# Optimization experiments

Hardware: AMD Instinct MI355X
Metric: run time of the kernel (lower is better)

Reference implementation:

```python
import jax, jax.numpy as jnp
import numpy as np

B = 8192       # batch
HID = 1024     # hidden_dim
HEADS = 8      # head_count
OBS, ACT, N_AGENTS = 128, 32, 4
ENC_IN = N_AGENTS * OBS + ACT   # 544
DEC_IN = (N_AGENTS - 1) * ACT   # 96


def _linear(key, fan_in, fan_out):
    k1, k2 = jax.random.split(key)
    lim = 1.0 / np.sqrt(fan_in)
    W = jax.random.uniform(k1, (fan_in, fan_out), minval=-lim, maxval=lim, dtype=jnp.float32)
    b = jax.random.uniform(k2, (fan_out,), minval=-lim, maxval=lim, dtype=jnp.float32)
    return W, b


def setup_inputs() -> dict:
    key = jax.random.key(0)
    ks = jax.random.split(key, 10)
    s = jax.random.normal(ks[0], (B, N_AGENTS * OBS), dtype=jnp.float32)
    a = jax.random.normal(ks[1], (B, N_AGENTS * ACT), dtype=jnp.float32)
    W_enc_in, b_enc_in = _linear(ks[2], ENC_IN, HID)   # encoder_input_fc
    W_dec_in, b_dec_in = _linear(ks[3], DEC_IN, HID)   # decoder_input_fc
    W_eh, b_eh = _linear(ks[4], HID, HID)              # fc_encoder_input
    head_ks = jax.random.split(ks[5], HEADS)
    Wb = [_linear(k, HID, HID) for k in head_ks]       # fc_encoder_heads
    W_heads = jnp.stack([w for w, _ in Wb], axis=0)    # [H, HID, HID]
    b_heads = jnp.stack([b for _, b in Wb], axis=0)    # [H, HID]
    W_dh, b_dh = _linear(ks[6], HID, HID)              # fc_decoder_input
    W1, b1 = _linear(ks[7], HID, HID)                  # fc1
    W2, b2 = _linear(ks[8], HID, 1)                    # fc2
    return {"s": s, "a": a,
            "W_enc_in": W_enc_in, "b_enc_in": b_enc_in,
            "W_dec_in": W_dec_in, "b_dec_in": b_dec_in,
            "W_eh": W_eh, "b_eh": b_eh,
            "W_heads": W_heads, "b_heads": b_heads,
            "W_dh": W_dh, "b_dh": b_dh,
            "W1": W1, "b1": b1, "W2": W2, "b2": b2}


def reference(s, a, W_enc_in, b_enc_in, W_dec_in, b_dec_in, W_eh, b_eh,
              W_heads, b_heads, W_dh, b_dh, W1, b1, W2, b2):
    relu = jax.nn.relu
    # agent id = 0: own action is a[:, :ACT], others' actions are a[:, ACT:]
    enc_input = jnp.concatenate([s, a[:, :ACT]], axis=1) @ W_enc_in + b_enc_in   # [B, HID]
    dec_input = a[:, ACT:] @ W_dec_in + b_dec_in                                 # [B, HID]
    # Attention_ATT_2
    encoder_h = relu(enc_input @ W_eh + b_eh)                                    # [B, HID]
    encoder_heads = relu(jnp.einsum('bd,hde->hbe', encoder_h, W_heads)
                         + b_heads[:, None, :])                                  # [H, B, HID]
    decoder_H = relu(dec_input @ W_dh + b_dh)                                    # [B, HID]
    scores = jnp.einsum('hbd,bd->bh', encoder_heads, decoder_H)                  # [B, H]
    attn = jax.nn.softmax(scores, axis=1)                                        # [B, H]
    context = jnp.einsum('hbd,bh->bd', encoder_heads, attn)                      # [B, HID]
    x = relu(context @ W1 + b1)
    q = x @ W2 + b2                                                              # [B, 1]
    return q
```

## Files before the change

kernel.cpp:

```cpp
#include <hip/hip_runtime.h>
#include <hip/hip_bf16.h>
#include <hip/hip_fp16.h>

#define BATCH   8192
#define HID     1024
#define HEADS   8
#define BC      2048

typedef unsigned int  u32;
typedef unsigned short u16;
typedef __attribute__((ext_vector_type(8))) short bf16x8;
typedef __attribute__((ext_vector_type(4))) float f32x4;

__device__ __forceinline__ u32 pack_hi2(u32 u0, u32 u1) {
    return (u0 >> 16) | (u1 & 0xFFFF0000u);
}
__device__ __forceinline__ void split1(float x, u16& h, u16& l) {
    const u32 u = __float_as_uint(x);
    h = (u16)(u >> 16);
    const float r = x - __uint_as_float(u & 0xFFFF0000u);
    l = (u16)(__float_as_uint(r) >> 16);
}
__device__ __forceinline__ void splitA4(float4 v, uint2& hi, uint2& lo) {
    u32 u0 = __float_as_uint(v.x), u1 = __float_as_uint(v.y),
        u2 = __float_as_uint(v.z), u3 = __float_as_uint(v.w);
    float r0 = v.x - __uint_as_float(u0 & 0xFFFF0000u);
    float r1 = v.y - __uint_as_float(u1 & 0xFFFF0000u);
    float r2 = v.z - __uint_as_float(u2 & 0xFFFF0000u);
    float r3 = v.w - __uint_as_float(u3 & 0xFFFF0000u);
    hi.x = pack_hi2(u0, u1);
    hi.y = pack_hi2(u2, u3);
    lo.x = pack_hi2(__float_as_uint(r0), __float_as_uint(r1));
    lo.y = pack_hi2(__float_as_uint(r2), __float_as_uint(r3));
}

__device__ __forceinline__ void gld16(const u16* g, u16* l) {
    __builtin_amdgcn_global_load_lds(
        (const __attribute__((address_space(1))) u32*)g,
        (__attribute__((address_space(3))) u32*)l, 16, 0, 0);
}

__global__ __launch_bounds__(256) void split_weight_kernel(
    const float* __restrict__ W, u16* __restrict__ hi, u16* __restrict__ lo,
    int K)
{
    const long long zoff = (long long)blockIdx.z * K * 1024;
    const int kt  = blockIdx.x;
    const int n0  = blockIdx.y * 128;
    const int tid = threadIdx.x;
    const int k   = tid >> 3;
    const int ng  = (tid & 7) * 16;
    const float* src = W + zoff + (long long)(kt * 32 + k) * 1024 + n0 + ng;
    u16* dh = hi + zoff + ((long long)kt * 1024 + n0) * 32 + k;
    u16* dl = lo + zoff + ((long long)kt * 1024 + n0) * 32 + k;
#pragma unroll
    for (int t = 0; t < 4; t++) {
        const float4 v = *(const float4*)(src + t * 4);
        u16 h0, l0, h1, l1, h2, l2, h3, l3;
        split1(v.x, h0, l0); split1(v.y, h1, l1);
        split1(v.z, h2, l2); split1(v.w, h3, l3);
        const int nb = (ng + t * 4) * 32;
        dh[nb]      = h0; dl[nb]      = l0;
        dh[nb + 32] = h1; dl[nb + 32] = l1;
        dh[nb + 64] = h2; dl[nb + 64] = l2;
        dh[nb + 96] = h3; dl[nb + 96] = l3;
    }
}

#define MFMA_GEOM \
    const int tid  = threadIdx.x; \
    const int lane = tid & 63; \
    const int wv   = tid >> 6; \
    const int wm   = wv >> 1, wn = wv & 1; \
    const int fr   = lane & 15; \
    const int fq   = lane >> 4; \
    const int fqx  = (fq ^ (fr & 3)) * 8; \
    const int lro  = (lane >> 2) * 32 + (((lane & 3) ^ ((lane >> 2) & 3)) * 8); \
    const int br0  = wv * 16; \
    const int br1  = 64 + wv * 16;

template <int RELU, int OUTP>
__global__ __launch_bounds__(256) void gemm_fast(
    const u16* __restrict__ Ahp, const u16* __restrict__ Alp, int MA, int moff,
    const u16* __restrict__ Bhp, const u16* __restrict__ Blp,
    const float* __restrict__ bias,
    float* __restrict__ Cf,
    u16* __restrict__ Chp, u16* __restrict__ Clp, int MC,
    int K)
{
    __shared__ alignas(16) u16 Ah[4096], Al[4096], Bh[4096], Bl[4096];
    MFMA_GEOM
    const int m0 = blockIdx.y * 128;
    const int n0 = blockIdx.x * 128;

    f32x4 acc[4][4];
#pragma unroll
    for (int i = 0; i < 4; i++)
#pragma unroll
        for (int j = 0; j < 4; j++) acc[i][j] = 0;

    const int KT = K >> 5;
    for (int kt = 0; kt < KT; kt++) {
        const u16* Ag  = Ahp + ((long long)kt * MA + moff + m0) * 32;
        const u16* Ag2 = Alp + ((long long)kt * MA + moff + m0) * 32;
        const u16* Bg  = Bhp + ((long long)kt * 1024 + n0) * 32;
        const u16* Bg2 = Blp + ((long long)kt * 1024 + n0) * 32;
        gld16(Ag  + br0 * 32 + lro, &Ah[br0 * 32]);
        gld16(Ag  + br1 * 32 + lro, &Ah[br1 * 32]);
        gld16(Ag2 + br0 * 32 + lro, &Al[br0 * 32]);
        gld16(Ag2 + br1 * 32 + lro, &Al[br1 * 32]);
        gld16(Bg  + br0 * 32 + lro, &Bh[br0 * 32]);
        gld16(Bg  + br1 * 32 + lro, &Bh[br1 * 32]);
        gld16(Bg2 + br0 * 32 + lro, &Bl[br0 * 32]);
        gld16(Bg2 + br1 * 32 + lro, &Bl[br1 * 32]);
        __syncthreads();

        bf16x8 ah[4], al[4], bh[4], bl[4];
#pragma unroll
        for (int i = 0; i < 4; i++) {
            const int off = (wm * 64 + i * 16 + fr) * 32 + fqx;
            ah[i] = *(const bf16x8*)&Ah[off];
            al[i] = *(const bf16x8*)&Al[off];
        }
#pragma unroll
        for (int j = 0; j < 4; j++) {
            const int off = (wn * 64 + j * 16 + fr) * 32 + fqx;
            bh[j] = *(const bf16x8*)&Bh[off];
            bl[j] = *(const bf16x8*)&Bl[off];
        }
#pragma unroll
        for (int i = 0; i < 4; i++)
#pragma unroll
            for (int j = 0; j < 4; j++) {
                acc[i][j] = __builtin_amdgcn_mfma_f32_16x16x32_bf16(ah[i], bh[j], acc[i][j], 0, 0, 0);
                acc[i][j] = __builtin_amdgcn_mfma_f32_16x16x32_bf16(ah[i], bl[j], acc[i][j], 0, 0, 0);
                acc[i][j] = __builtin_amdgcn_mfma_f32_16x16x32_bf16(al[i], bh[j], acc[i][j], 0, 0, 0);
            }
        __syncthreads();
    }

#pragma unroll
    for (int j = 0; j < 4; j++) {
        const int n = n0 + wn * 64 + j * 16 + fr;
        const float bb = bias[n];
#pragma unroll
        for (int i = 0; i < 4; i++) {
#pragma unroll
            for (int r = 0; r < 4; r++) {
                const int m = m0 + wm * 64 + i * 16 + fq * 4 + r;
                float v = acc[i][j][r] + bb;
                if (RELU) v = fmaxf(v, 0.0f);
                if (OUTP) {
                    u16 h, l;
                    split1(v, h, l);
                    const long long d = ((long long)(n >> 5) * MC + moff + m) * 32 + (n & 31);
                    Chp[d] = h;
                    Clp[d] = l;
                } else {
                    Cf[(long long)m * 1024 + n] = v;
                }
            }
        }
    }
}

template <int RELU>
__global__ __launch_bounds__(256) void gemm_cvt(
    const float* __restrict__ src1, int lda1, int kofs1,
    const float* __restrict__ src2, int lda2, int ksplit,
    const u16* __restrict__ Bhp, const u16* __restrict__ Blp,
    const float* __restrict__ bias,
    u16* __restrict__ Chp, u16* __restrict__ Clp, int MC,
    int K)
{
    __shared__ alignas(16) u16 Ah[4096], Al[4096], Bh[4096], Bl[4096];
    MFMA_GEOM
    const int m0  = blockIdx.y * 128;
    const int n0  = blockIdx.x * 128;
    const int ar  = tid >> 3;
    const int akq = tid & 7;
    const int awoff = (( (akq >> 1) ^ (ar & 3) ) * 8) + (akq & 1) * 4;

    f32x4 acc[4][4];
#pragma unroll
    for (int i = 0; i < 4; i++)
#pragma unroll
        for (int j = 0; j < 4; j++) acc[i][j] = 0;

    const int KT = K >> 5;
    for (int kt = 0; kt < KT; kt++) {
        const int k0 = kt * 32;
        const float* srcp; int ldk, kc;
        if (k0 < ksplit) { srcp = src1; ldk = lda1; kc = k0 + kofs1; }
        else             { srcp = src2; ldk = lda2; kc = k0 - ksplit; }

        const u16* Bg  = Bhp + ((long long)kt * 1024 + n0) * 32;
        const u16* Bg2 = Blp + ((long long)kt * 1024 + n0) * 32;
        gld16(Bg  + br0 * 32 + lro, &Bh[br0 * 32]);
        gld16(Bg  + br1 * 32 + lro, &Bh[br1 * 32]);
        gld16(Bg2 + br0 * 32 + lro, &Bl[br0 * 32]);
        gld16(Bg2 + br1 * 32 + lro, &Bl[br1 * 32]);

#pragma unroll
        for (int it = 0; it < 4; it++) {
            const int row = ar + it * 32;
            const float4 v = *(const float4*)(srcp + (long long)(m0 + row) * ldk + kc + akq * 4);
            uint2 hi, lo;
            splitA4(v, hi, lo);
            *(uint2*)&Ah[row * 32 + awoff] = hi;
            *(uint2*)&Al[row * 32 + awoff] = lo;
        }
        __syncthreads();

        bf16x8 ah[4], al[4], bh[4], bl[4];
#pragma unroll
        for (int i = 0; i < 4; i++) {
            const int off = (wm * 64 + i * 16 + fr) * 32 + fqx;
            ah[i] = *(const bf16x8*)&Ah[off];
            al[i] = *(const bf16x8*)&Al[off];
        }
#pragma unroll
        for (int j = 0; j < 4; j++) {
            const int off = (wn * 64 + j * 16 + fr) * 32 + fqx;
            bh[j] = *(const bf16x8*)&Bh[off];
            bl[j] = *(const bf16x8*)&Bl[off];
        }
#pragma unroll
        for (int i = 0; i < 4; i++)
#pragma unroll
            for (int j = 0; j < 4; j++) {
                acc[i][j] = __builtin_amdgcn_mfma_f32_16x16x32_bf16(ah[i], bh[j], acc[i][j], 0, 0, 0);
                acc[i][j] = __builtin_amdgcn_mfma_f32_16x16x32_bf16(ah[i], bl[j], acc[i][j], 0, 0, 0);
                acc[i][j] = __builtin_amdgcn_mfma_f32_16x16x32_bf16(al[i], bh[j], acc[i][j], 0, 0, 0);
            }
        __syncthreads();
    }

#pragma unroll
    for (int j = 0; j < 4; j++) {
        const int n = n0 + wn * 64 + j * 16 + fr;
        const float bb = bias[n];
#pragma unroll
        for (int i = 0; i < 4; i++) {
#pragma unroll
            for (int r = 0; r < 4; r++) {
                const int m = m0 + wm * 64 + i * 16 + fq * 4 + r;
                float v = acc[i][j][r] + bb;
                if (RELU) v = fmaxf(v, 0.0f);
                u16 h, l;
                split1(v, h, l);
                const long long d = ((long long)(n >> 5) * MC + m) * 32 + (n & 31);
                Chp[d] = h;
                Clp[d] = l;
            }
        }
    }
}

__global__ __launch_bounds__(256) void heads_kernel(
    const u16* __restrict__ Ahp, const u16* __restrict__ Alp, int MA, int moff,
    const u16* __restrict__ Whp, const u16* __restrict__ Wlp,
    const float* __restrict__ b_heads,
    const float* __restrict__ decH,
    __half* __restrict__ headsb,
    float* __restrict__ scoresp)
{
    __shared__ alignas(16) u16 Ah[4096], Al[4096], Bh[4096], Bl[4096];
    __shared__ float scred[2][128];
    MFMA_GEOM
    const int h = blockIdx.z;
    const u16* Bhp = Whp + (long long)h * 1024 * 1024;
    const u16* Blp = Wlp + (long long)h * 1024 * 1024;
    const float* bias = b_heads + h * 1024;
    const int m0 = blockIdx.y * 128;
    const int n0 = blockIdx.x * 128;

    f32x4 acc[4][4];
#pragma unroll
    for (int i = 0; i < 4; i++)
#pragma unroll
        for (int j = 0; j < 4; j++) acc[i][j] = 0;

    for (int kt = 0; kt < 32; kt++) {
        const u16* Ag  = Ahp + ((long long)kt * MA + moff + m0) * 32;
        const u16* Ag2 = Alp + ((long long)kt * MA + moff + m0) * 32;
        const u16* Bg  = Bhp + ((long long)kt * 1024 + n0) * 32;
        const u16* Bg2 = Blp + ((long long)kt * 1024 + n0) * 32;
        gld16(Ag  + br0 * 32 + lro, &Ah[br0 * 32]);
        gld16(Ag  + br1 * 32 + lro, &Ah[br1 * 32]);
        gld16(Ag2 + br0 * 32 + lro, &Al[br0 * 32]);
        gld16(Ag2 + br1 * 32 + lro, &Al[br1 * 32]);
        gld16(Bg  + br0 * 32 + lro, &Bh[br0 * 32]);
        gld16(Bg  + br1 * 32 + lro, &Bh[br1 * 32]);
        gld16(Bg2 + br0 * 32 + lro, &Bl[br0 * 32]);
        gld16(Bg2 + br1 * 32 + lro, &Bl[br1 * 32]);
        __syncthreads();

        bf16x8 ah[4], al[4], bh[4], bl[4];
#pragma unroll
        for (int i = 0; i < 4; i++) {
            const int off = (wm * 64 + i * 16 + fr) * 32 + fqx;
            ah[i] = *(const bf16x8*)&Ah[off];
            al[i] = *(const bf16x8*)&Al[off];
        }
#pragma unroll
        for (int j = 0; j < 4; j++) {
            const int off = (wn * 64 + j * 16 + fr) * 32 + fqx;
            bh[j] = *(const bf16x8*)&Bh[off];
            bl[j] = *(const bf16x8*)&Bl[off];
        }
#pragma unroll
        for (int i = 0; i < 4; i++)
#pragma unroll
            for (int j = 0; j < 4; j++) {
                acc[i][j] = __builtin_amdgcn_mfma_f32_16x16x32_bf16(ah[i], bh[j], acc[i][j], 0, 0, 0);
                acc[i][j] = __builtin_amdgcn_mfma_f32_16x16x32_bf16(ah[i], bl[j], acc[i][j], 0, 0, 0);
                acc[i][j] = __builtin_amdgcn_mfma_f32_16x16x32_bf16(al[i], bh[j], acc[i][j], 0, 0, 0);
            }
        __syncthreads();
    }

    float part[4][4];
#pragma unroll
    for (int i = 0; i < 4; i++)
#pragma unroll
        for (int r = 0; r < 4; r++) part[i][r] = 0.0f;

#pragma unroll
    for (int j = 0; j < 4; j++) {
        const int n = n0 + wn * 64 + j * 16 + fr;
        const float bb = bias[n];
#pragma unroll
        for (int i = 0; i < 4; i++) {
#pragma unroll
            for (int r = 0; r < 4; r++) {
                const int b_loc = m0 + wm * 64 + i * 16 + fq * 4 + r;
                const float v = fmaxf(acc[i][j][r] + bb, 0.0f);
                headsb[((long long)b_loc * HEADS + h) * 1024 + n] = __float2half(v);
                part[i][r] = fmaf(v, decH[(long long)b_loc * 1024 + n], part[i][r]);
            }
        }
    }
#pragma unroll
    for (int off = 1; off < 16; off <<= 1)
#pragma unroll
        for (int i = 0; i < 4; i++)
#pragma unroll
            for (int r = 0; r < 4; r++)
                part[i][r] += __shfl_xor(part[i][r], off, 64);

    if (fr == 0) {
#pragma unroll
        for (int i = 0; i < 4; i++)
#pragma unroll
            for (int r = 0; r < 4; r++)
                scred[wn][wm * 64 + i * 16 + fq * 4 + r] = part[i][r];
    }
    __syncthreads();
    if (tid < 128) {
        const float sv = scred[0][tid] + scred[1][tid];
        scoresp[(long long)(h * 8 + blockIdx.x) * BC + m0 + tid] = sv;
    }
}

__global__ __launch_bounds__(256) void softmax_kernel(
    const float* __restrict__ scoresp, float* __restrict__ attn)
{
    const int b = blockIdx.x * 256 + threadIdx.x;
    float sc[HEADS];
#pragma unroll
    for (int h = 0; h < HEADS; h++) {
        float s = 0.0f;
#pragma unroll
        for (int nt = 0; nt < 8; nt++)
            s += scoresp[(long long)(h * 8 + nt) * BC + b];
        sc[h] = s;
    }
    float mx = sc[0];
#pragma unroll
    for (int h = 1; h < HEADS; h++) mx = fmaxf(mx, sc[h]);
    float e[HEADS], sum = 0.0f;
#pragma unroll
    for (int h = 0; h < HEADS; h++) { e[h] = __expf(sc[h] - mx); sum += e[h]; }
    const float inv = 1.0f / sum;
#pragma unroll
    for (int h = 0; h < HEADS; h++) attn[(long long)b * HEADS + h] = e[h] * inv;
}

__global__ __launch_bounds__(256) void context_kernel(
    const __half* __restrict__ headsb, const float* __restrict__ attn,
    u16* __restrict__ ctx_hi, u16* __restrict__ ctx_lo, int MC, int row0)
{
    const int b = blockIdx.x;
    const int d = threadIdx.x * 4;
    float w[HEADS];
#pragma unroll
    for (int h = 0; h < HEADS; h++) w[h] = attn[(long long)b * HEADS + h];
    float4 acc = make_float4(0.f, 0.f, 0.f, 0.f);
#pragma unroll
    for (int h = 0; h < HEADS; h++) {
        const __half2* hp = (const __half2*)(headsb + ((long long)b * HEADS + h) * 1024 + d);
        const float2 f0 = __half22float2(hp[0]);
        const float2 f1 = __half22float2(hp[1]);
        acc.x = fmaf(w[h], f0.x, acc.x);
        acc.y = fmaf(w[h], f0.y, acc.y);
        acc.z = fmaf(w[h], f1.x, acc.z);
        acc.w = fmaf(w[h], f1.y, acc.w);
    }
    uint2 hi, lo;
    splitA4(acc, hi, lo);
    const long long off = ((long long)(d >> 5) * MC + row0 + b) * 32 + (d & 31);
    *(uint2*)(ctx_hi + off) = hi;
    *(uint2*)(ctx_lo + off) = lo;
}

__global__ __launch_bounds__(256) void fc2_kernel(
    const float* __restrict__ x, const float* __restrict__ W2,
    const float* __restrict__ b2, float* __restrict__ q)
{
    const int b   = blockIdx.x;
    const int tid = threadIdx.x;
    __shared__ float red[4];

    const float4 xv = *(const float4*)(x + (long long)b * 1024 + tid * 4);
    const float4 wv = *(const float4*)(W2 + tid * 4);
    float p = xv.x * wv.x + xv.y * wv.y + xv.z * wv.z + xv.w * wv.w;
#pragma unroll
    for (int off = 32; off > 0; off >>= 1) p += __shfl_down(p, off, 64);
    if ((tid & 63) == 0) red[tid >> 6] = p;
    __syncthreads();
    if (tid == 0) q[b] = red[0] + red[1] + red[2] + red[3] + b2[0];
}

extern "C" void kernel_launch(void* const* d_in, const int* in_sizes, int n_in,
                              void* d_out, int out_size, void* d_ws, size_t ws_size,
                              hipStream_t stream)
{
    const float* s        = (const float*)d_in[0];
    const float* a        = (const float*)d_in[1];
    const float* W_enc_in = (const float*)d_in[2];
    const float* b_enc_in = (const float*)d_in[3];
    const float* W_dec_in = (const float*)d_in[4];
    const float* b_dec_in = (const float*)d_in[5];
    const float* W_eh     = (const float*)d_in[6];
    const float* b_eh     = (const float*)d_in[7];
    const float* W_heads  = (const float*)d_in[8];
    const float* b_heads  = (const float*)d_in[9];
    const float* W_dh     = (const float*)d_in[10];
    const float* b_dh     = (const float*)d_in[11];
    const float* W1       = (const float*)d_in[12];
    const float* b1       = (const float*)d_in[13];
    const float* W2       = (const float*)d_in[14];
    const float* b2       = (const float*)d_in[15];
    float* q_out = (float*)d_out;

    u16* P = (u16*)d_ws;
    u16* enc_hi = P; P += 557056;
    u16* enc_lo = P; P += 557056;
    u16* dec_hi = P; P += 98304;
    u16* dec_lo = P; P += 98304;
    u16* eh_hi  = P; P += 1048576;
    u16* eh_lo  = P; P += 1048576;
    u16* dh_hi  = P; P += 1048576;
    u16* dh_lo  = P; P += 1048576;
    u16* w1_hi  = P; P += 1048576;
    u16* w1_lo  = P; P += 1048576;
    u16* wh_hi  = P; P += 8388608;
    u16* wh_lo  = P; P += 8388608;
    char* act = (char*)P;

    const dim3 blk(256);

    split_weight_kernel<<<dim3(17, 8, 1), blk, 0, stream>>>(W_enc_in, enc_hi, enc_lo, 544);
    split_weight_kernel<<<dim3(3, 8, 1), blk, 0, stream>>>(W_dec_in, dec_hi, dec_lo, 96);
    split_weight_kernel<<<dim3(32, 8, 1), blk, 0, stream>>>(W_eh, eh_hi, eh_lo, 1024);
    split_weight_kernel<<<dim3(32, 8, 1), blk, 0, stream>>>(W_dh, dh_hi, dh_lo, 1024);
    split_weight_kernel<<<dim3(32, 8, 1), blk, 0, stream>>>(W1, w1_hi, w1_lo, 1024);
    split_weight_kernel<<<dim3(32, 8, 8), blk, 0, stream>>>(W_heads, wh_hi, wh_lo, 1024);

    const bool high = (ws_size >= 150011904ULL);

    if (high) {
        u16*    bufA_hi = (u16*)act;
        u16*    bufA_lo = bufA_hi + 8388608;
        __half* headsb  = (__half*)act;
        u16*    encH_hi = (u16*)(act + 33554432);
        u16*    encH_lo = encH_hi + 8388608;
        float*  decH    = (float*)(act + 2LL * 33554432);
        float*  scoresp = (float*)(act + 3LL * 33554432);
        float*  attnb   = scoresp + 64LL * BC;

        const dim3 gg(8, 64, 1);
        gemm_cvt<0><<<gg, blk, 0, stream>>>(s, 512, 0, a, 128, 512,
            enc_hi, enc_lo, b_enc_in, bufA_hi, bufA_lo, 8192, 544);
        gemm_fast<1, 1><<<gg, blk, 0, stream>>>(bufA_hi, bufA_lo, 8192, 0,
            eh_hi, eh_lo, b_eh, nullptr, encH_hi, encH_lo, 8192, 1024);
        gemm_cvt<0><<<gg, blk, 0, stream>>>(a, 128, 32, a, 128, 1 << 28,
            dec_hi, dec_lo, b_dec_in, bufA_hi, bufA_lo, 8192, 96);
        gemm_fast<1, 0><<<gg, blk, 0, stream>>>(bufA_hi, bufA_lo, 8192, 0,
            dh_hi, dh_lo, b_dh, decH, nullptr, nullptr, 0, 1024);

        for (int c = 0; c < BATCH / BC; c++) {
            heads_kernel<<<dim3(8, BC / 128, 8), blk, 0, stream>>>(
                encH_hi, encH_lo, 8192, c * BC, wh_hi, wh_lo, b_heads,
                decH + (long long)c * BC * 1024, headsb, scoresp);
            softmax_kernel<<<dim3(BC / 256), blk, 0, stream>>>(scoresp, attnb);
            context_kernel<<<dim3(BC), blk, 0, stream>>>(
                headsb, attnb, encH_hi, encH_lo, 8192, c * BC);
        }
        gemm_fast<1, 0><<<gg, blk, 0, stream>>>(encH_hi, encH_lo, 8192, 0,
            w1_hi, w1_lo, b1, decH, nullptr, nullptr, 0, 1024);
        fc2_kernel<<<dim3(BATCH), blk, 0, stream>>>(decH, W2, b2, q_out);
    } else {
        __half* headsb  = (__half*)act;
        u16*    bufA_hi = (u16*)act;
        u16*    bufA_lo = bufA_hi + 2097152;
        u16*    encH_hi = (u16*)(act + 33554432);
        u16*    encH_lo = encH_hi + 2097152;
        float*  decH    = (float*)(act + 33554432 + 8388608);
        float*  scoresp = (float*)(act + 33554432 + 2LL * 8388608);
        float*  attnb   = scoresp + 64LL * BC;

        const dim3 gg(8, BC / 128, 1);
        for (int c = 0; c < BATCH / BC; c++) {
            const float* sC = s + (long long)c * BC * 512;
            const float* aC = a + (long long)c * BC * 128;
            gemm_cvt<0><<<gg, blk, 0, stream>>>(sC, 512, 0, aC, 128, 512,
                enc_hi, enc_lo, b_enc_in, bufA_hi, bufA_lo, BC, 544);
            gemm_fast<1, 1><<<gg, blk, 0, stream>>>(bufA_hi, bufA_lo, BC, 0,
                eh_hi, eh_lo, b_eh, nullptr, encH_hi, encH_lo, BC, 1024);
            gemm_cvt<0><<<gg, blk, 0, stream>>>(aC, 128, 32, aC, 128, 1 << 28,
                dec_hi, dec_lo, b_dec_in, bufA_hi, bufA_lo, BC, 96);
            gemm_fast<1, 0><<<gg, blk, 0, stream>>>(bufA_hi, bufA_lo, BC, 0,
                dh_hi, dh_lo, b_dh, decH, nullptr, nullptr, 0, 1024);
            heads_kernel<<<dim3(8, BC / 128, 8), blk, 0, stream>>>(
                encH_hi, encH_lo, BC, 0, wh_hi, wh_lo, b_heads,
                decH, headsb, scoresp);
            softmax_kernel<<<dim3(BC / 256), blk, 0, stream>>>(scoresp, attnb);
            context_kernel<<<dim3(BC), blk, 0, stream>>>(
                headsb, attnb, encH_hi, encH_lo, BC, 0);
            gemm_fast<1, 0><<<gg, blk, 0, stream>>>(encH_hi, encH_lo, BC, 0,
                w1_hi, w1_lo, b1, decH, nullptr, nullptr, 0, 1024);
            fc2_kernel<<<dim3(BC), blk, 0, stream>>>(decH, W2, b2, q_out + (long long)c * BC);
        }
    }
}
```

Before: 828.3 us.

## Load MFMA fragments directly from global memory with register double-buffering

Drops the shared-memory staging and the barriers from gemm_fast and heads_kernel. Each wave now loads its bf16 hi/lo MFMA fragments straight from the packed global layout into registers. Two fragment sets are used so the next k-step's loads overlap the current MFMAs. In exchange, cross-wave data reuse through LDS is lost (each A/B fragment is fetched by two waves), global and L2 traffic rises, and register pressure grows. The loop also assumes KT is even and issues one redundant wrap-around load at the end.

After: 1.130 ms. +36.4%, slower.

```diff
diff --git a/kernel.cpp b/kernel.cpp
--- a/kernel.cpp
+++ b/kernel.cpp
@@ -67,17 +67,46 @@
     }
 }
 
-#define MFMA_GEOM \
+struct Frags {
+    bf16x8 ah[4], al[4], bh[4], bl[4];
+};
+
+__device__ __forceinline__ void load_set(
+    Frags& f,
+    const u16* __restrict__ Ahp, const u16* __restrict__ Alp,
+    const u16* __restrict__ Bhp, const u16* __restrict__ Blp,
+    long long abase, long long bbase)
+{
+#pragma unroll
+    for (int i = 0; i < 4; i++) {
+        f.ah[i] = *(const bf16x8*)(Ahp + abase + i * 512);
+        f.al[i] = *(const bf16x8*)(Alp + abase + i * 512);
+        f.bh[i] = *(const bf16x8*)(Bhp + bbase + i * 512);
+        f.bl[i] = *(const bf16x8*)(Blp + bbase + i * 512);
+    }
+}
+
+__device__ __forceinline__ void mfma_set(f32x4 acc[4][4], const Frags& f)
+{
+#pragma unroll
+    for (int i = 0; i < 4; i++)
+#pragma unroll
+        for (int j = 0; j < 4; j++) {
+            acc[i][j] = __builtin_amdgcn_mfma_f32_16x16x32_bf16(f.ah[i], f.bh[j], acc[i][j], 0, 0, 0);
+            acc[i][j] = __builtin_amdgcn_mfma_f32_16x16x32_bf16(f.ah[i], f.bl[j], acc[i][j], 0, 0, 0);
+            acc[i][j] = __builtin_amdgcn_mfma_f32_16x16x32_bf16(f.al[i], f.bh[j], acc[i][j], 0, 0, 0);
+        }
+}
+
+#define DIRECT_GEOM \
     const int tid  = threadIdx.x; \
     const int lane = tid & 63; \
     const int wv   = tid >> 6; \
     const int wm   = wv >> 1, wn = wv & 1; \
     const int fr   = lane & 15; \
     const int fq   = lane >> 4; \
-    const int fqx  = (fq ^ (fr & 3)) * 8; \
-    const int lro  = (lane >> 2) * 32 + (((lane & 3) ^ ((lane >> 2) & 3)) * 8); \
-    const int br0  = wv * 16; \
-    const int br1  = 64 + wv * 16;
+    const int m0   = blockIdx.y * 128; \
+    const int n0   = blockIdx.x * 128;
 
 template <int RELU, int OUTP>
 __global__ __launch_bounds__(256) void gemm_fast(
@@ -88,10 +117,7 @@
     u16* __restrict__ Chp, u16* __restrict__ Clp, int MC,
     int K)
 {
-    __shared__ alignas(16) u16 Ah[4096], Al[4096], Bh[4096], Bl[4096];
-    MFMA_GEOM
-    const int m0 = blockIdx.y * 128;
-    const int n0 = blockIdx.x * 128;
+    DIRECT_GEOM
 
     f32x4 acc[4][4];
 #pragma unroll
@@ -99,44 +125,21 @@
 #pragma unroll
         for (int j = 0; j < 4; j++) acc[i][j] = 0;
 
+    const long long astep = (long long)MA * 32;
+    const long long bstep = 1024LL * 32;
+    const long long a0 = ((long long)moff + m0 + wm * 64 + fr) * 32 + fq * 8;
+    const long long b0 = ((long long)n0 + wn * 64 + fr) * 32 + fq * 8;
+
     const int KT = K >> 5;
-    for (int kt = 0; kt < KT; kt++) {
-        const u16* Ag  = Ahp + ((long long)kt * MA + moff + m0) * 32;
-        const u16* Ag2 = Alp + ((long long)kt * MA + moff + m0) * 32;
-        const u16* Bg  = Bhp + ((long long)kt * 1024 + n0) * 32;
-        const u16* Bg2 = Blp + ((long long)kt * 1024 + n0) * 32;
-        gld16(Ag  + br0 * 32 + lro, &Ah[br0 * 32]);
-        gld16(Ag  + br1 * 32 + lro, &Ah[br1 * 32]);
-        gld16(Ag2 + br0 * 32 + lro, &Al[br0 * 32]);
-        gld16(Ag2 + br1 * 32 + lro, &Al[br1 * 32]);
-        gld16(Bg  + br0 * 32 + lro, &Bh[br0 * 32]);
-        gld16(Bg  + br1 * 32 + lro, &Bh[br1 * 32]);
-        gld16(Bg2 + br0 * 32 + lro, &Bl[br0 * 32]);
-        gld16(Bg2 + br1 * 32 + lro, &Bl[br1 * 32]);
-        __syncthreads();
-
-        bf16x8 ah[4], al[4], bh[4], bl[4];
-#pragma unroll
-        for (int i = 0; i < 4; i++) {
-            const int off = (wm * 64 + i * 16 + fr) * 32 + fqx;
-            ah[i] = *(const bf16x8*)&Ah[off];
-            al[i] = *(const bf16x8*)&Al[off];
-        }
-#pragma unroll
-        for (int j = 0; j < 4; j++) {
-            const int off = (wn * 64 + j * 16 + fr) * 32 + fqx;
-            bh[j] = *(const bf16x8*)&Bh[off];
-            bl[j] = *(const bf16x8*)&Bl[off];
-        }
-#pragma unroll
-        for (int i = 0; i < 4; i++)
-#pragma unroll
-            for (int j = 0; j < 4; j++) {
-                acc[i][j] = __builtin_amdgcn_mfma_f32_16x16x32_bf16(ah[i], bh[j], acc[i][j], 0, 0, 0);
-                acc[i][j] = __builtin_amdgcn_mfma_f32_16x16x32_bf16(ah[i], bl[j], acc[i][j], 0, 0, 0);
-                acc[i][j] = __builtin_amdgcn_mfma_f32_16x16x32_bf16(al[i], bh[j], acc[i][j], 0, 0, 0);
-            }
-        __syncthreads();
+    Frags f0, f1;
+    load_set(f0, Ahp, Alp, Bhp, Blp, a0, b0);
+    for (int kt = 0; kt < KT; kt += 2) {
+        load_set(f1, Ahp, Alp, Bhp, Blp,
+                 a0 + (kt + 1) * astep, b0 + (kt + 1) * bstep);
+        mfma_set(acc, f0);
+        const int k2 = (kt + 2 < KT) ? kt + 2 : 0;
+        load_set(f0, Ahp, Alp, Bhp, Blp, a0 + k2 * astep, b0 + k2 * bstep);
+        mfma_set(acc, f1);
     }
 
 #pragma unroll
@@ -174,12 +177,14 @@
     int K)
 {
     __shared__ alignas(16) u16 Ah[4096], Al[4096], Bh[4096], Bl[4096];
-    MFMA_GEOM
-    const int m0  = blockIdx.y * 128;
-    const int n0  = blockIdx.x * 128;
-    const int ar  = tid >> 3;
-    const int akq = tid & 7;
-    const int awoff = (( (akq >> 1) ^ (ar & 3) ) * 8) + (akq & 1) * 4;
+    DIRECT_GEOM
+    const int fqx  = (fq ^ (fr & 3)) * 8;
+    const int lro  = (lane >> 2) * 32 + (((lane & 3) ^ ((lane >> 2) & 3)) * 8);
+    const int br0  = wv * 16;
+    const int br1  = 64 + wv * 16;
+    const int ar   = tid >> 3;
+    const int akq  = tid & 7;
+    const int awoff = (((akq >> 1) ^ (ar & 3)) * 8) + (akq & 1) * 4;
 
     f32x4 acc[4][4];
 #pragma unroll
@@ -265,15 +270,12 @@
     __half* __restrict__ headsb,
     float* __restrict__ scoresp)
 {
-    __shared__ alignas(16) u16 Ah[4096], Al[4096], Bh[4096], Bl[4096];
     __shared__ float scred[2][128];
-    MFMA_GEOM
+    DIRECT_GEOM
     const int h = blockIdx.z;
     const u16* Bhp = Whp + (long long)h * 1024 * 1024;
     const u16* Blp = Wlp + (long long)h * 1024 * 1024;
     const float* bias = b_heads + h * 1024;
-    const int m0 = blockIdx.y * 128;
-    const int n0 = blockIdx.x * 128;
 
     f32x4 acc[4][4];
 #pragma unroll
@@ -281,43 +283,20 @@
 #pragma unroll
         for (int j = 0; j < 4; j++) acc[i][j] = 0;
 
-    for (int kt = 0; kt < 32; kt++) {
-        const u16* Ag  = Ahp + ((long long)kt * MA + moff + m0) * 32;
-        const u16* Ag2 = Alp + ((long long)kt * MA + moff + m0) * 32;
-        const u16* Bg  = Bhp + ((long long)kt * 1024 + n0) * 32;
-        const u16* Bg2 = Blp + ((long long)kt * 1024 + n0) * 32;
-        gld16(Ag  + br0 * 32 + lro, &Ah[br0 * 32]);
-        gld16(Ag  + br1 * 32 + lro, &Ah[br1 * 32]);
-        gld16(Ag2 + br0 * 32 + lro, &Al[br0 * 32]);
-        gld16(Ag2 + br1 * 32 + lro, &Al[br1 * 32]);
-        gld16(Bg  + br0 * 32 + lro, &Bh[br0 * 32]);
-        gld16(Bg  + br1 * 32 + lro, &Bh[br1 * 32]);
-        gld16(Bg2 + br0 * 32 + lro, &Bl[br0 * 32]);
-        gld16(Bg2 + br1 * 32 + lro, &Bl[br1 * 32]);
-        __syncthreads();
-
-        bf16x8 ah[4], al[4], bh[4], bl[4];
-#pragma unroll
-        for (int i = 0; i < 4; i++) {
-            const int off = (wm * 64 + i * 16 + fr) * 32 + fqx;
-            ah[i] = *(const bf16x8*)&Ah[off];
-            al[i] = *(const bf16x8*)&Al[off];
-        }
-#pragma unroll
-        for (int j = 0; j < 4; j++) {
-            const int off = (wn * 64 + j * 16 + fr) * 32 + fqx;
-            bh[j] = *(const bf16x8*)&Bh[off];
-            bl[j] = *(const bf16x8*)&Bl[off];
-        }
-#pragma unroll
-        for (int i = 0; i < 4; i++)
-#pragma unroll
-            for (int j = 0; j < 4; j++) {
-                acc[i][j] = __builtin_amdgcn_mfma_f32_16x16x32_bf16(ah[i], bh[j], acc[i][j], 0, 0, 0);
-                acc[i][j] = __builtin_amdgcn_mfma_f32_16x16x32_bf16(ah[i], bl[j], acc[i][j], 0, 0, 0);
-                acc[i][j] = __builtin_amdgcn_mfma_f32_16x16x32_bf16(al[i], bh[j], acc[i][j], 0, 0, 0);
-            }
-        __syncthreads();
+    const long long astep = (long long)MA * 32;
+    const long long bstep = 1024LL * 32;
+    const long long a0 = ((long long)moff + m0 + wm * 64 + fr) * 32 + fq * 8;
+    const long long b0 = ((long long)n0 + wn * 64 + fr) * 32 + fq * 8;
+
+    Frags f0, f1;
+    load_set(f0, Ahp, Alp, Bhp, Blp, a0, b0);
+    for (int kt = 0; kt < 32; kt += 2) {
+        load_set(f1, Ahp, Alp, Bhp, Blp,
+                 a0 + (kt + 1) * astep, b0 + (kt + 1) * bstep);
+        mfma_set(acc, f0);
+        const int k2 = (kt + 2 < 32) ? kt + 2 : 0;
+        load_set(f0, Ahp, Alp, Bhp, Blp, a0 + k2 * astep, b0 + k2 * bstep);
+        mfma_set(acc, f1);
     }
 
     float part[4][4];
```
